# Performance work log

Hardware: AMD Instinct MI355X
Metric: run time of the kernel (lower is better)

Reference implementation:

```python
import jax, jax.numpy as jnp
import numpy as np

N, M, E, C, F, K = 10000, 20000, 160000, 128, 128, 3
R_CORRECTION = 1.0  # UpsampleModule passes 1 to DPOConv


def setup_inputs() -> dict:
    key = jax.random.key(0)
    ks = jax.random.split(key, 8)
    x = jax.random.normal(ks[0], (N, C), dtype=jnp.float32)
    pos = jax.random.uniform(ks[1], (N, 2), dtype=jnp.float32)
    pos_skip = jax.random.uniform(ks[2], (M, 2), dtype=jnp.float32)
    edge_index = jax.random.randint(ks[3], (2, E), 0, N, dtype=jnp.int64)
    W_conv = jax.random.normal(ks[4], (4 * C, F), dtype=jnp.float32) * 0.02
    b_conv = jnp.zeros((F,), dtype=jnp.float32)
    W2 = jax.random.normal(ks[5], (F, F), dtype=jnp.float32) * 0.02
    b2 = jnp.zeros((F,), dtype=jnp.float32)
    return {"x": x, "pos": pos, "pos_skip": pos_skip, "edge_index": edge_index,
            "W_conv": W_conv, "b_conv": b_conv, "W2": W2, "b2": b2}


def _dpo_conv(x, pos, edge_index, W_conv, b_conv):
    src, dst = edge_index[0], edge_index[1]  # PyG flow: j=source, i=target
    v_j, v_i = x[src], x[dst]                # [E, C]
    diff = pos[dst] - pos[src]               # pos_i - pos_j, [E, 2]
    r2 = jnp.sum(diff * diff, axis=-1)       # [E]
    scale = R_CORRECTION / (r2 + 0.01)       # [E]
    dx = diff[:, 0] * scale
    dy = diff[:, 1] * scale
    v_diff = v_i - v_j
    f = jnp.concatenate([v_diff * dx[:, None], v_diff * dy[:, None], v_j], axis=1)  # [E, 3C]
    agg = jax.ops.segment_sum(f, dst, num_segments=N)
    cnt = jax.ops.segment_sum(jnp.ones((E,), x.dtype), dst, num_segments=N)
    agg = agg / jnp.maximum(cnt, 1.0)[:, None]  # aggr='mean'
    h = jnp.concatenate([agg, x], axis=1) @ W_conv + b_conv  # [N, F]
    return h


def _knn_interpolate(h, pos, pos_skip, k):
    # squared distances target->source, [M, N]
    d2 = jnp.sum((pos_skip[:, None, :] - pos[None, :, :]) ** 2, axis=-1)
    neg_d, idx = jax.lax.top_k(-d2, k)         # k nearest, [M, k]
    w = 1.0 / jnp.maximum(-neg_d, 1e-16)       # inverse squared-distance weights
    return jnp.sum(w[:, :, None] * h[idx], axis=1) / jnp.sum(w, axis=1)[:, None]


def reference(x, pos, pos_skip, edge_index, W_conv, b_conv, W2, b2):
    h = _dpo_conv(x, pos, edge_index, W_conv, b_conv)
    h = jax.nn.elu(h)
    h = jax.nn.elu(h @ W2 + b2)
    return _knn_interpolate(h, pos, pos_skip, K)  # [M, F]
```

## Files before the change

kernel.cpp:

```cpp
#include <hip/hip_runtime.h>
#include <hip/hip_bf16.h>
#include <math.h>
#include <float.h>
#include <stdint.h>

#define N_NODES 10000
#define M_PTS   20000
#define E_EDGES 160000
#define C_CH    128
#define F_CH    128
#define G_GRID  64
#define N_CELLS (G_GRID*G_GRID)
#define NPB     16
#define ECAP    64
#define CCAP    24
#define A_STRIDE 520
#define H_STRIDE 136
#define N_TILES (N_NODES / NPB)
#define W1SZ (4*C_CH*F_CH)
#define W2SZ (F_CH*F_CH)

typedef __attribute__((ext_vector_type(8))) short short8;
typedef __attribute__((ext_vector_type(4))) float f32x4;

__device__ inline ushort f2bf(float v) {
    __hip_bfloat16 b = __float2bfloat16(v);
    return *reinterpret_cast<ushort*>(&b);
}
__device__ inline float bf2f(ushort u) {
    __hip_bfloat16 b = *reinterpret_cast<__hip_bfloat16*>(&u);
    return __bfloat162float(b);
}
__device__ inline float eluf(float v) { return (v > 0.f) ? v : expm1f(v); }
__device__ inline void insert3(uint64_t key, uint64_t& k0, uint64_t& k1, uint64_t& k2) {
    bool lt2 = key < k2, lt1 = key < k1, lt0 = key < k0;
    k2 = lt1 ? k1 : (lt2 ? key : k2);
    k1 = lt0 ? k0 : (lt1 ? key : k1);
    k0 = lt0 ? key : k0;
}

__global__ __launch_bounds__(256) void build_kernel(const int* __restrict__ ei,
    const float* __restrict__ pos, int* __restrict__ ecur, int* __restrict__ ccur,
    int4* __restrict__ edata, int4* __restrict__ cdata,
    const float* __restrict__ Wc, const float* __restrict__ W2,
    ushort* __restrict__ Wct_h, ushort* __restrict__ Wct_l,
    ushort* __restrict__ W2t_h, ushort* __restrict__ W2t_l)
{
    int i = blockIdx.x * 256 + threadIdx.x;
    if (i < E_EDGES) {
        int src = ei[i];
        int dst = ei[E_EDGES + i];
        float dxv = pos[2*dst]     - pos[2*src];
        float dyv = pos[2*dst + 1] - pos[2*src + 1];
        float r2 = dxv*dxv + dyv*dyv;
        float scale = 1.0f / (r2 + 0.01f);
        int slot = atomicAdd(&ecur[dst], 1);
        if (slot < ECAP)
            edata[dst*ECAP + slot] = make_int4(src, __float_as_int(dxv*scale),
                                               __float_as_int(dyv*scale), 0);
    } else if (i < E_EDGES + N_NODES) {
        int j = i - E_EDGES;
        float px = pos[2*j], py = pos[2*j+1];
        int cx = min(max((int)(px * G_GRID), 0), G_GRID - 1);
        int cy = min(max((int)(py * G_GRID), 0), G_GRID - 1);
        int c = cy * G_GRID + cx;
        int slot = atomicAdd(&ccur[c], 1);
        if (slot < CCAP)
            cdata[c*CCAP + slot] = make_int4(__float_as_int(px), __float_as_int(py), j, 0);
    } else if (i < E_EDGES + N_NODES + W1SZ) {
        int j = i - (E_EDGES + N_NODES);
        int n = j >> 9, k = j & 511;
        float v = Wc[k*F_CH + n];
        ushort h = f2bf(v);
        Wct_h[j] = h;
        Wct_l[j] = f2bf(v - bf2f(h));
    } else if (i < E_EDGES + N_NODES + W1SZ + W2SZ) {
        int j = i - (E_EDGES + N_NODES + W1SZ);
        int n = j >> 7, k = j & 127;
        float v = W2[k*F_CH + n];
        ushort h = f2bf(v);
        W2t_h[j] = h;
        W2t_l[j] = f2bf(v - bf2f(h));
    }
}

__global__ __launch_bounds__(1024, 8) void mega_kernel(const float* __restrict__ x,
    const int* __restrict__ ecur, const int4* __restrict__ edata,
    const ushort* __restrict__ Wct_h, const ushort* __restrict__ Wct_l,
    const ushort* __restrict__ W2t_h, const ushort* __restrict__ W2t_l,
    const float* __restrict__ bc, const float* __restrict__ b2,
    float* __restrict__ h2out,
    const float* __restrict__ pos_skip, const int* __restrict__ ccur,
    const int4* __restrict__ cdata,
    int* __restrict__ knn_idx, float* __restrict__ knn_w)
{
    __shared__ alignas(16) ushort sA_h[NPB * A_STRIDE];
    __shared__ alignas(16) ushort sA_l[NPB * A_STRIDE];
    __shared__ alignas(16) ushort sH_h[NPB * H_STRIDE];
    __shared__ alignas(16) ushort sH_l[NPB * H_STRIDE];

    const int bid = blockIdx.x;
    const int tid = threadIdx.x;
    const int lane = tid & 63;
    const int wave = tid >> 6;

    if (bid % 5 == 4) {
        int gt = (bid / 5) * 1024 + tid;
        if (gt >= M_PTS * 8) return;
        int t = gt >> 3;
        int sub = gt & 7;
        float tx = pos_skip[2*t], ty = pos_skip[2*t+1];
        const float h = 1.0f / G_GRID;
        int cx = min(max((int)(tx * G_GRID), 0), G_GRID - 1);
        int cy = min(max((int)(ty * G_GRID), 0), G_GRID - 1);

        uint64_t m0 = UINT64_MAX, m1 = UINT64_MAX, m2 = UINT64_MAX;
        bool done;
        {
            uint64_t k0 = UINT64_MAX, k1 = UINT64_MAX, k2 = UINT64_MAX;
            int cc[4];
            int qq[4];
            #pragma unroll
            for (int s = 0; s < 4; s++) {
                int cidx = sub + 8*s;
                int yy = cy + cidx / 5 - 2;
                int xx = cx + cidx % 5 - 2;
                bool ok = (cidx < 25) && (yy >= 0) && (yy < G_GRID) &&
                          (xx >= 0) && (xx < G_GRID);
                cc[s] = ok ? (yy * G_GRID + xx) : -1;
            }
            #pragma unroll
            for (int s = 0; s < 4; s++)
                qq[s] = (cc[s] >= 0) ? min(ccur[cc[s]], CCAP) : 0;
            #pragma unroll
            for (int s = 0; s < 4; s++) {
                const int4* cb = cdata + (size_t)(cc[s] < 0 ? 0 : cc[s]) * CCAP;
                int q = qq[s];
                int p = 0;
                for (; p + 1 < q; p += 2) {
                    int4 sa = cb[p];
                    int4 sb = cb[p+1];
                    float dax = __fadd_rn(__int_as_float(sa.x), -tx);
                    float day = __fadd_rn(__int_as_float(sa.y), -ty);
                    float da  = __fadd_rn(__fmul_rn(dax, dax), __fmul_rn(day, day));
                    insert3(((uint64_t)__float_as_uint(da) << 32) | (uint32_t)sa.z, k0, k1, k2);
                    float dbx = __fadd_rn(__int_as_float(sb.x), -tx);
                    float dby = __fadd_rn(__int_as_float(sb.y), -ty);
                    float db  = __fadd_rn(__fmul_rn(dbx, dbx), __fmul_rn(dby, dby));
                    insert3(((uint64_t)__float_as_uint(db) << 32) | (uint32_t)sb.z, k0, k1, k2);
                }
                if (p < q) {
                    int4 sa = cb[p];
                    float dax = __fadd_rn(__int_as_float(sa.x), -tx);
                    float day = __fadd_rn(__int_as_float(sa.y), -ty);
                    float da  = __fadd_rn(__fmul_rn(dax, dax), __fmul_rn(day, day));
                    insert3(((uint64_t)__float_as_uint(da) << 32) | (uint32_t)sa.z, k0, k1, k2);
                }
            }
            m0 = k0; m1 = k1; m2 = k2;
            #pragma unroll
            for (int m = 1; m <= 4; m <<= 1) {
                uint64_t p0 = __shfl_xor((unsigned long long)m0, m, 64);
                uint64_t p1 = __shfl_xor((unsigned long long)m1, m, 64);
                uint64_t p2 = __shfl_xor((unsigned long long)m2, m, 64);
                insert3(p0, m0, m1, m2);
                insert3(p1, m0, m1, m2);
                insert3(p2, m0, m1, m2);
            }
            float d2cur = __uint_as_float((uint32_t)(m2 >> 32));
            done = (d2cur < (2.0f * h) * (2.0f * h) * 0.99999f);
        }

        if (!done) {
            uint64_t k0 = UINT64_MAX, k1 = UINT64_MAX, k2 = UINT64_MAX;
            m0 = UINT64_MAX; m1 = UINT64_MAX; m2 = UINT64_MAX;
            for (int r = 0; ; r++) {
                if (r >= 2) {
                    m0 = k0; m1 = k1; m2 = k2;
                    #pragma unroll
                    for (int m = 1; m <= 4; m <<= 1) {
                        uint64_t p0 = __shfl_xor((unsigned long long)m0, m, 64);
                        uint64_t p1 = __shfl_xor((unsigned long long)m1, m, 64);
                        uint64_t p2 = __shfl_xor((unsigned long long)m2, m, 64);
                        insert3(p0, m0, m1, m2);
                        insert3(p1, m0, m1, m2);
                        insert3(p2, m0, m1, m2);
                    }
                    float bound = ((r - 1) * h) * ((r - 1) * h) * 0.99999f;
                    float d2cur = __uint_as_float((uint32_t)(m2 >> 32));
                    if (d2cur < bound || r >= G_GRID) break;
                }
                int x0 = max(cx - r, 0), x1 = min(cx + r, G_GRID - 1);
                int y0 = max(cy - r, 0), y1 = min(cy + r, G_GRID - 1);
                int cidx = 0;
                for (int yy = y0; yy <= y1; yy++) {
                    bool yedge = (yy == cy - r) || (yy == cy + r);
                    for (int xx = x0; xx <= x1; xx++) {
                        if (r > 0 && !yedge && xx != cx - r && xx != cx + r) continue;
                        if ((cidx++ & 7) != sub) continue;
                        int c = yy * G_GRID + xx;
                        int pc = min(ccur[c], CCAP);
                        const int4* cb = cdata + c*CCAP;
                        for (int p = 0; p < pc; p++) {
                            int4 sp = cb[p];
                            float ddx = __fadd_rn(__int_as_float(sp.x), -tx);
                            float ddy = __fadd_rn(__int_as_float(sp.y), -ty);
                            float dd = __fadd_rn(__fmul_rn(ddx, ddx), __fmul_rn(ddy, ddy));
                            uint64_t key = ((uint64_t)__float_as_uint(dd) << 32) | (uint32_t)sp.z;
                            insert3(key, k0, k1, k2);
                        }
                    }
                }
            }
        }

        if (sub == 0) {
            float d0 = __uint_as_float((uint32_t)(m0 >> 32));
            float d1 = __uint_as_float((uint32_t)(m1 >> 32));
            float d2 = __uint_as_float((uint32_t)(m2 >> 32));
            float w0 = 1.0f / fmaxf(d0, 1e-16f);
            float w1 = 1.0f / fmaxf(d1, 1e-16f);
            float w2 = 1.0f / fmaxf(d2, 1e-16f);
            float wsum = w0 + w1 + w2;
            knn_idx[t*3+0] = (int)(uint32_t)m0;
            knn_idx[t*3+1] = (int)(uint32_t)m1;
            knn_idx[t*3+2] = (int)(uint32_t)m2;
            knn_w[t*3+0] = w0 / wsum;
            knn_w[t*3+1] = w1 / wsum;
            knn_w[t*3+2] = w2 / wsum;
        }
        return;
    }

    const int agg_id = bid - bid / 5;
    if (agg_id >= N_TILES) return;
    const int nodeBase = agg_id * NPB;
    const float2* xv = (const float2*)x;

    {
        const int rr = wave;
        int node = nodeBase + rr;
        float2 xi = xv[(size_t)node*64 + lane];
        int cnt = ecur[node];
        int m = min(cnt, ECAP);
        int4 er = edata[(size_t)node*ECAP + lane];
        double a1x = 0., a1y = 0., a2x = 0., a2y = 0., a3x = 0., a3y = 0.;
        int p = 0;
        for (; p + 3 < m; p += 4) {
            int s0 = __shfl(er.x, p);     int s1 = __shfl(er.x, p+1);
            int s2 = __shfl(er.x, p+2);   int s3 = __shfl(er.x, p+3);
            float dx0 = __int_as_float(__shfl(er.y, p));
            float dy0 = __int_as_float(__shfl(er.z, p));
            float dx1 = __int_as_float(__shfl(er.y, p+1));
            float dy1 = __int_as_float(__shfl(er.z, p+1));
            float dx2 = __int_as_float(__shfl(er.y, p+2));
            float dy2 = __int_as_float(__shfl(er.z, p+2));
            float dx3 = __int_as_float(__shfl(er.y, p+3));
            float dy3 = __int_as_float(__shfl(er.z, p+3));
            float2 x0 = xv[(size_t)s0*64 + lane];
            float2 x1 = xv[(size_t)s1*64 + lane];
            float2 x2 = xv[(size_t)s2*64 + lane];
            float2 x3 = xv[(size_t)s3*64 + lane];
            float vx0 = xi.x - x0.x, vy0 = xi.y - x0.y;
            float vx1 = xi.x - x1.x, vy1 = xi.y - x1.y;
            float vx2 = xi.x - x2.x, vy2 = xi.y - x2.y;
            float vx3 = xi.x - x3.x, vy3 = xi.y - x3.y;
            a1x += (double)(vx0*dx0); a1y += (double)(vy0*dx0);
            a2x += (double)(vx0*dy0); a2y += (double)(vy0*dy0);
            a3x += (double)x0.x;      a3y += (double)x0.y;
            a1x += (double)(vx1*dx1); a1y += (double)(vy1*dx1);
            a2x += (double)(vx1*dy1); a2y += (double)(vy1*dy1);
            a3x += (double)x1.x;      a3y += (double)x1.y;
            a1x += (double)(vx2*dx2); a1y += (double)(vy2*dx2);
            a2x += (double)(vx2*dy2); a2y += (double)(vy2*dy2);
            a3x += (double)x2.x;      a3y += (double)x2.y;
            a1x += (double)(vx3*dx3); a1y += (double)(vy3*dx3);
            a2x += (double)(vx3*dy3); a2y += (double)(vy3*dy3);
            a3x += (double)x3.x;      a3y += (double)x3.y;
        }
        for (; p < m; p++) {
            int s = __shfl(er.x, p);
            float dxe = __int_as_float(__shfl(er.y, p));
            float dye = __int_as_float(__shfl(er.z, p));
            float2 xj = xv[(size_t)s*64 + lane];
            float vx = xi.x - xj.x, vy = xi.y - xj.y;
            a1x += (double)(vx*dxe); a1y += (double)(vy*dxe);
            a2x += (double)(vx*dye); a2y += (double)(vy*dye);
            a3x += (double)xj.x;     a3y += (double)xj.y;
        }
        float inv = 1.0f / fmaxf((float)cnt, 1.0f);
        float vals[4][2] = {{(float)a1x*inv, (float)a1y*inv},
                            {(float)a2x*inv, (float)a2y*inv},
                            {(float)a3x*inv, (float)a3y*inv},
                            {xi.x, xi.y}};
        int b = rr * A_STRIDE;
        int c0 = 2*lane;
        #pragma unroll
        for (int seg = 0; seg < 4; seg++) {
            ushort hx = f2bf(vals[seg][0]), hy = f2bf(vals[seg][1]);
            ushort lx = f2bf(vals[seg][0] - bf2f(hx)), ly = f2bf(vals[seg][1] - bf2f(hy));
            *(uint*)&sA_h[b + seg*128 + c0] = (uint)hx | ((uint)hy << 16);
            *(uint*)&sA_l[b + seg*128 + c0] = (uint)lx | ((uint)ly << 16);
        }
    }
    __syncthreads();

    const int col16 = lane & 15;
    const int quad  = lane >> 4;
    const int row   = col16;
    const int ncol  = (wave & 7)*16 + col16;

    if (wave < 8) {
        const float bcv = bc[ncol];
        f32x4 acc = {0,0,0,0};
        for (int ks = 0; ks < 16; ks++) {
            int kb = ks*32 + quad*8;
            short8 ah = *(const short8*)&sA_h[row*A_STRIDE + kb];
            short8 al = *(const short8*)&sA_l[row*A_STRIDE + kb];
            short8 bh = *(const short8*)(Wct_h + (size_t)ncol*512 + kb);
            short8 bl = *(const short8*)(Wct_l + (size_t)ncol*512 + kb);
            acc = __builtin_amdgcn_mfma_f32_16x16x32_bf16(ah, bh, acc, 0, 0, 0);
            acc = __builtin_amdgcn_mfma_f32_16x16x32_bf16(ah, bl, acc, 0, 0, 0);
            acc = __builtin_amdgcn_mfma_f32_16x16x32_bf16(al, bh, acc, 0, 0, 0);
        }
        #pragma unroll
        for (int r = 0; r < 4; r++) {
            int rr = quad*4 + r;
            float v = eluf(acc[r] + bcv);
            ushort hh = f2bf(v);
            sH_h[rr*H_STRIDE + ncol] = hh;
            sH_l[rr*H_STRIDE + ncol] = f2bf(v - bf2f(hh));
        }
    }
    __syncthreads();

    if (wave < 8) {
        const float b2v = b2[ncol];
        f32x4 acc2 = {0,0,0,0};
        for (int ks = 0; ks < 4; ks++) {
            int kb = ks*32 + quad*8;
            short8 ah = *(const short8*)&sH_h[row*H_STRIDE + kb];
            short8 al = *(const short8*)&sH_l[row*H_STRIDE + kb];
            short8 bh = *(const short8*)(W2t_h + ncol*128 + kb);
            short8 bl = *(const short8*)(W2t_l + ncol*128 + kb);
            acc2 = __builtin_amdgcn_mfma_f32_16x16x32_bf16(ah, bh, acc2, 0, 0, 0);
            acc2 = __builtin_amdgcn_mfma_f32_16x16x32_bf16(ah, bl, acc2, 0, 0, 0);
            acc2 = __builtin_amdgcn_mfma_f32_16x16x32_bf16(al, bh, acc2, 0, 0, 0);
        }
        #pragma unroll
        for (int r = 0; r < 4; r++) {
            int node = nodeBase + quad*4 + r;
            float v = eluf(acc2[r] + b2v);
            h2out[(size_t)node*F_CH + ncol] = v;
        }
    }
}

__global__ __launch_bounds__(256) void gather_kernel(const float* __restrict__ h2,
    const int* __restrict__ knn_idx, const float* __restrict__ knn_w,
    float* __restrict__ out)
{
    int m = blockIdx.x * 4 + (threadIdx.x >> 6);
    int lane = threadIdx.x & 63;
    const float2* h2v = (const float2*)h2;
    int j0 = knn_idx[m*3+0], j1 = knn_idx[m*3+1], j2 = knn_idx[m*3+2];
    float w0 = knn_w[m*3+0], w1 = knn_w[m*3+1], w2 = knn_w[m*3+2];
    float2 a = h2v[(size_t)j0*64 + lane], b = h2v[(size_t)j1*64 + lane], c = h2v[(size_t)j2*64 + lane];
    float2 v;
    v.x = w0*a.x + w1*b.x + w2*c.x;
    v.y = w0*a.y + w1*b.y + w2*c.y;
    ((float2*)out)[(size_t)m*64 + lane] = v;
}

extern "C" void kernel_launch(void* const* d_in, const int* in_sizes, int n_in,
                              void* d_out, int out_size, void* d_ws, size_t ws_size,
                              hipStream_t stream) {
    const float* x        = (const float*)d_in[0];
    const float* pos      = (const float*)d_in[1];
    const float* pos_skip = (const float*)d_in[2];
    const int*   ei       = (const int*)  d_in[3];
    const float* Wc       = (const float*)d_in[4];
    const float* bc       = (const float*)d_in[5];
    const float* W2       = (const float*)d_in[6];
    const float* b2       = (const float*)d_in[7];
    float* out = (float*)d_out;

    char* ws = (char*)d_ws;
    size_t off = 0;
    auto alloc = [&](size_t bytes) {
        void* p = ws + off;
        off = (off + bytes + 255) & ~(size_t)255;
        return p;
    };
    int*    ecur    = (int*)   alloc((size_t)N_NODES * 4);
    int*    ccur    = (int*)   alloc((size_t)N_CELLS * 4);
    size_t  cur_bytes = (size_t)((char*)ccur - (char*)ecur) + (size_t)N_CELLS * 4;
    int4*   edata   = (int4*)  alloc((size_t)N_NODES * ECAP * 16);
    int4*   cdata   = (int4*)  alloc((size_t)N_CELLS * CCAP * 16);
    float*  h2      = (float*) alloc((size_t)N_NODES * F_CH * 4);
    int*    knn_idx = (int*)   alloc((size_t)M_PTS * 3 * 4);
    float*  knn_w   = (float*) alloc((size_t)M_PTS * 3 * 4);
    ushort* Wct_h   = (ushort*)alloc((size_t)F_CH * 512 * 2);
    ushort* Wct_l   = (ushort*)alloc((size_t)F_CH * 512 * 2);
    ushort* W2t_h   = (ushort*)alloc((size_t)F_CH * 128 * 2);
    ushort* W2t_l   = (ushort*)alloc((size_t)F_CH * 128 * 2);

    hipMemsetAsync(ecur, 0, cur_bytes, stream);
    const int TOT = E_EDGES + N_NODES + W1SZ + W2SZ;
    build_kernel<<<(TOT + 255) / 256, 256, 0, stream>>>(ei, pos, ecur, ccur, edata, cdata,
                                                        Wc, W2, Wct_h, Wct_l, W2t_h, W2t_l);
    mega_kernel<<<785, 1024, 0, stream>>>(x, ecur, edata,
        Wct_h, Wct_l, W2t_h, W2t_l, bc, b2, h2,
        pos_skip, ccur, cdata, knn_idx, knn_w);
    gather_kernel<<<M_PTS / 4, 256, 0, stream>>>(h2, knn_idx, knn_w, out);
}
```

Baseline: 139.5 us.

## Split dense GEMMs out of mega kernel into a 64-row tiled GEMM kernel

The aggregation stage now writes the split-bf16 feature matrix to global memory instead of shared memory. A new GEMM kernel computes both linear layers on 64-row tiles, which lets each weight fragment serve four row tiles instead of one. The old code used only 8 of 16 waves for the 16-row GEMM and reloaded the weights per tile. The cost is an extra global round trip for the A matrix (about 20 MB) and an extra kernel launch.

```diff
diff --git a/kernel.cpp b/kernel.cpp
--- a/kernel.cpp
+++ b/kernel.cpp
@@ -14,8 +14,9 @@
 #define NPB     16
 #define ECAP    64
 #define CCAP    24
-#define A_STRIDE 520
-#define H_STRIDE 136
+#define AROWS   10048
+#define GROWS   64
+#define S_STRIDE 136
 #define N_TILES (N_NODES / NPB)
 #define W1SZ (4*C_CH*F_CH)
 #define W2SZ (F_CH*F_CH)
@@ -86,19 +87,11 @@
 
 __global__ __launch_bounds__(1024, 8) void mega_kernel(const float* __restrict__ x,
     const int* __restrict__ ecur, const int4* __restrict__ edata,
-    const ushort* __restrict__ Wct_h, const ushort* __restrict__ Wct_l,
-    const ushort* __restrict__ W2t_h, const ushort* __restrict__ W2t_l,
-    const float* __restrict__ bc, const float* __restrict__ b2,
-    float* __restrict__ h2out,
+    ushort* __restrict__ Ah, ushort* __restrict__ Al,
     const float* __restrict__ pos_skip, const int* __restrict__ ccur,
     const int4* __restrict__ cdata,
     int* __restrict__ knn_idx, float* __restrict__ knn_w)
 {
-    __shared__ alignas(16) ushort sA_h[NPB * A_STRIDE];
-    __shared__ alignas(16) ushort sA_l[NPB * A_STRIDE];
-    __shared__ alignas(16) ushort sH_h[NPB * H_STRIDE];
-    __shared__ alignas(16) ushort sH_l[NPB * H_STRIDE];
-
     const int bid = blockIdx.x;
     const int tid = threadIdx.x;
     const int lane = tid & 63;
@@ -293,65 +286,113 @@
                             {(float)a2x*inv, (float)a2y*inv},
                             {(float)a3x*inv, (float)a3y*inv},
                             {xi.x, xi.y}};
-        int b = rr * A_STRIDE;
-        int c0 = 2*lane;
+        uint* Ah32 = (uint*)Ah;
+        uint* Al32 = (uint*)Al;
+        size_t b32 = (size_t)node*256;
         #pragma unroll
         for (int seg = 0; seg < 4; seg++) {
             ushort hx = f2bf(vals[seg][0]), hy = f2bf(vals[seg][1]);
             ushort lx = f2bf(vals[seg][0] - bf2f(hx)), ly = f2bf(vals[seg][1] - bf2f(hy));
-            *(uint*)&sA_h[b + seg*128 + c0] = (uint)hx | ((uint)hy << 16);
-            *(uint*)&sA_l[b + seg*128 + c0] = (uint)lx | ((uint)ly << 16);
-        }
-    }
-    __syncthreads();
-
+            Ah32[b32 + seg*64 + lane] = (uint)hx | ((uint)hy << 16);
+            Al32[b32 + seg*64 + lane] = (uint)lx | ((uint)ly << 16);
+        }
+    }
+}
+
+__global__ __launch_bounds__(512) void gemm_kernel(
+    const ushort* __restrict__ Ah, const ushort* __restrict__ Al,
+    const ushort* __restrict__ Wct_h, const ushort* __restrict__ Wct_l,
+    const ushort* __restrict__ W2t_h, const ushort* __restrict__ W2t_l,
+    const float* __restrict__ bc, const float* __restrict__ b2,
+    float* __restrict__ h2out)
+{
+    __shared__ alignas(16) ushort sP0[GROWS * S_STRIDE];
+    __shared__ alignas(16) ushort sP1[GROWS * S_STRIDE];
+
+    const int tid   = threadIdx.x;
+    const int lane  = tid & 63;
+    const int wave  = tid >> 6;
     const int col16 = lane & 15;
     const int quad  = lane >> 4;
-    const int row   = col16;
-    const int ncol  = (wave & 7)*16 + col16;
-
-    if (wave < 8) {
-        const float bcv = bc[ncol];
-        f32x4 acc = {0,0,0,0};
-        for (int ks = 0; ks < 16; ks++) {
+    const int ncol  = wave*16 + col16;
+    const int rowBase = blockIdx.x * GROWS;
+
+    const float bcv = bc[ncol];
+    f32x4 acc0 = {0,0,0,0}, acc1 = {0,0,0,0}, acc2 = {0,0,0,0}, acc3 = {0,0,0,0};
+
+    const int srow = tid >> 3;
+    const int sseg = tid & 7;
+
+    for (int kc = 0; kc < 4; kc++) {
+        if (kc) __syncthreads();
+        {
+            size_t g = (size_t)(rowBase + srow)*512 + kc*128 + sseg*16;
+            int l = srow*S_STRIDE + sseg*16;
+            *(short8*)&sP0[l]     = *(const short8*)&Ah[g];
+            *(short8*)&sP0[l + 8] = *(const short8*)&Ah[g + 8];
+            *(short8*)&sP1[l]     = *(const short8*)&Al[g];
+            *(short8*)&sP1[l + 8] = *(const short8*)&Al[g + 8];
+        }
+        __syncthreads();
+        for (int ks = 0; ks < 4; ks++) {
             int kb = ks*32 + quad*8;
-            short8 ah = *(const short8*)&sA_h[row*A_STRIDE + kb];
-            short8 al = *(const short8*)&sA_l[row*A_STRIDE + kb];
-            short8 bh = *(const short8*)(Wct_h + (size_t)ncol*512 + kb);
-            short8 bl = *(const short8*)(Wct_l + (size_t)ncol*512 + kb);
-            acc = __builtin_amdgcn_mfma_f32_16x16x32_bf16(ah, bh, acc, 0, 0, 0);
-            acc = __builtin_amdgcn_mfma_f32_16x16x32_bf16(ah, bl, acc, 0, 0, 0);
-            acc = __builtin_amdgcn_mfma_f32_16x16x32_bf16(al, bh, acc, 0, 0, 0);
-        }
+            short8 bh = *(const short8*)(Wct_h + (size_t)ncol*512 + kc*128 + kb);
+            short8 bl = *(const short8*)(Wct_l + (size_t)ncol*512 + kc*128 + kb);
+            #pragma unroll
+            for (int rt = 0; rt < 4; rt++) {
+                int ar = (rt*16 + col16)*S_STRIDE + kb;
+                short8 ah = *(const short8*)&sP0[ar];
+                short8 al = *(const short8*)&sP1[ar];
+                f32x4 a = (rt==0)?acc0:(rt==1)?acc1:(rt==2)?acc2:acc3;
+                a = __builtin_amdgcn_mfma_f32_16x16x32_bf16(ah, bh, a, 0, 0, 0);
+                a = __builtin_amdgcn_mfma_f32_16x16x32_bf16(ah, bl, a, 0, 0, 0);
+                a = __builtin_amdgcn_mfma_f32_16x16x32_bf16(al, bh, a, 0, 0, 0);
+                if (rt==0) acc0 = a; else if (rt==1) acc1 = a; else if (rt==2) acc2 = a; else acc3 = a;
+            }
+        }
+    }
+    __syncthreads();
+
+    #pragma unroll
+    for (int rt = 0; rt < 4; rt++) {
+        f32x4 a = (rt==0)?acc0:(rt==1)?acc1:(rt==2)?acc2:acc3;
         #pragma unroll
         for (int r = 0; r < 4; r++) {
-            int rr = quad*4 + r;
-            float v = eluf(acc[r] + bcv);
+            int row = rt*16 + quad*4 + r;
+            float v = eluf(a[r] + bcv);
             ushort hh = f2bf(v);
-            sH_h[rr*H_STRIDE + ncol] = hh;
-            sH_l[rr*H_STRIDE + ncol] = f2bf(v - bf2f(hh));
+            sP0[row*S_STRIDE + ncol] = hh;
+            sP1[row*S_STRIDE + ncol] = f2bf(v - bf2f(hh));
         }
     }
     __syncthreads();
 
-    if (wave < 8) {
-        const float b2v = b2[ncol];
-        f32x4 acc2 = {0,0,0,0};
-        for (int ks = 0; ks < 4; ks++) {
-            int kb = ks*32 + quad*8;
-            short8 ah = *(const short8*)&sH_h[row*H_STRIDE + kb];
-            short8 al = *(const short8*)&sH_l[row*H_STRIDE + kb];
-            short8 bh = *(const short8*)(W2t_h + ncol*128 + kb);
-            short8 bl = *(const short8*)(W2t_l + ncol*128 + kb);
-            acc2 = __builtin_amdgcn_mfma_f32_16x16x32_bf16(ah, bh, acc2, 0, 0, 0);
-            acc2 = __builtin_amdgcn_mfma_f32_16x16x32_bf16(ah, bl, acc2, 0, 0, 0);
-            acc2 = __builtin_amdgcn_mfma_f32_16x16x32_bf16(al, bh, acc2, 0, 0, 0);
-        }
+    const float b2v = b2[ncol];
+    f32x4 c0 = {0,0,0,0}, c1 = {0,0,0,0}, c2 = {0,0,0,0}, c3 = {0,0,0,0};
+    for (int ks = 0; ks < 4; ks++) {
+        int kb = ks*32 + quad*8;
+        short8 bh = *(const short8*)(W2t_h + ncol*128 + kb);
+        short8 bl = *(const short8*)(W2t_l + ncol*128 + kb);
+        #pragma unroll
+        for (int rt = 0; rt < 4; rt++) {
+            int ar = (rt*16 + col16)*S_STRIDE + kb;
+            short8 ah = *(const short8*)&sP0[ar];
+            short8 al = *(const short8*)&sP1[ar];
+            f32x4 a = (rt==0)?c0:(rt==1)?c1:(rt==2)?c2:c3;
+            a = __builtin_amdgcn_mfma_f32_16x16x32_bf16(ah, bh, a, 0, 0, 0);
+            a = __builtin_amdgcn_mfma_f32_16x16x32_bf16(ah, bl, a, 0, 0, 0);
+            a = __builtin_amdgcn_mfma_f32_16x16x32_bf16(al, bh, a, 0, 0, 0);
+            if (rt==0) c0 = a; else if (rt==1) c1 = a; else if (rt==2) c2 = a; else c3 = a;
+        }
+    }
+    #pragma unroll
+    for (int rt = 0; rt < 4; rt++) {
+        f32x4 a = (rt==0)?c0:(rt==1)?c1:(rt==2)?c2:c3;
         #pragma unroll
         for (int r = 0; r < 4; r++) {
-            int node = nodeBase + quad*4 + r;
-            float v = eluf(acc2[r] + b2v);
-            h2out[(size_t)node*F_CH + ncol] = v;
+            int node = rowBase + rt*16 + quad*4 + r;
+            if (node < N_NODES)
+                h2out[(size_t)node*F_CH + ncol] = eluf(a[r] + b2v);
         }
     }
 }
@@ -404,13 +445,16 @@
     ushort* Wct_l   = (ushort*)alloc((size_t)F_CH * 512 * 2);
     ushort* W2t_h   = (ushort*)alloc((size_t)F_CH * 128 * 2);
     ushort* W2t_l   = (ushort*)alloc((size_t)F_CH * 128 * 2);
+    ushort* Ah      = (ushort*)alloc((size_t)AROWS * 512 * 2);
+    ushort* Al      = (ushort*)alloc((size_t)AROWS * 512 * 2);
 
     hipMemsetAsync(ecur, 0, cur_bytes, stream);
     const int TOT = E_EDGES + N_NODES + W1SZ + W2SZ;
     build_kernel<<<(TOT + 255) / 256, 256, 0, stream>>>(ei, pos, ecur, ccur, edata, cdata,
                                                         Wc, W2, Wct_h, Wct_l, W2t_h, W2t_l);
-    mega_kernel<<<785, 1024, 0, stream>>>(x, ecur, edata,
-        Wct_h, Wct_l, W2t_h, W2t_l, bc, b2, h2,
+    mega_kernel<<<785, 1024, 0, stream>>>(x, ecur, edata, Ah, Al,
         pos_skip, ccur, cdata, knn_idx, knn_w);
+    gemm_kernel<<<(AROWS / GROWS), 512, 0, stream>>>(Ah, Al, Wct_h, Wct_l, W2t_h, W2t_l,
+                                                     bc, b2, h2);
     gather_kernel<<<M_PTS / 4, 256, 0, stream>>>(h2, knn_idx, knn_w, out);
 }
```

New measurement: 140.0 us. No clear change (+0.3%).
